# Performance work log

Hardware: AMD Instinct MI355X
Metric: run time of the kernel (lower is better)

The kernel has to match this reference:

```python
import jax, jax.numpy as jnp
import numpy as np

T, B, C = 4, 2, 128
LT, LH, LW = 8, 32, 32
NUM_HEADS = 8
HEAD_DIM = C // NUM_HEADS
THETA = 0.7
V_TH = 1.0
TAU = 2.0  # spikingjelly LIFNode default tau
N_WIN = (2, 2, 2)
TOPK = 4
EPS = 1e-5
ATAN_ALPHA = 2.0  # spikingjelly surrogate.ATan default


@jax.custom_vjp
def spike(x):
    return (x >= 0.0).astype(x.dtype)

def _spike_fwd(x):
    return spike(x), x

def _spike_bwd(x, g):
    s = (jnp.pi / 2.0) * ATAN_ALPHA * x
    return (g * (ATAN_ALPHA / 2.0) / (1.0 + s * s),)

spike.defvjp(_spike_fwd, _spike_bwd)


def lif(x_seq):
    """Multi-step LIF: v'=v+(x-v)/tau, spike at v>=V_TH, hard reset to 0 (detached)."""
    def step(v, x):
        v = v + (x - v) / TAU
        s = spike(v - V_TH)
        v = v * (1.0 - jax.lax.stop_gradient(s))  # detach_reset, v_reset=0
        return v, s
    _, s_seq = jax.lax.scan(step, jnp.zeros_like(x_seq[0]), x_seq)
    return s_seq


def bn(x, gamma, beta):
    # BatchNorm3d(track_running_stats=False) on [T*B, C, D, H, W]: batch stats per channel
    mean = x.mean(axis=(0, 1, 3, 4, 5), keepdims=True)
    var = x.var(axis=(0, 1, 3, 4, 5), keepdims=True)
    shp = (1, 1, -1, 1, 1, 1)
    return (x - mean) * jax.lax.rsqrt(var + EPS) * gamma.reshape(shp) + beta.reshape(shp)


def conv3d(x, w, pad):
    t, b = x.shape[:2]
    y = jax.lax.conv_general_dilated(
        x.reshape((t * b,) + x.shape[2:]), w,
        window_strides=(1, 1, 1), padding=[(pad, pad)] * 3,
        dimension_numbers=('NCDHW', 'OIDHW', 'NCDHW'))
    return y.reshape((t, b) + y.shape[1:])


def cdc_t(x, w):
    out = conv3d(x, w, 1)
    # central-difference temporal term: 1x1x1 conv with summed first/last temporal slices
    kd = w[:, :, 0].sum((-1, -2)) + w[:, :, 2].sum((-1, -2))  # [O, I]
    return out - THETA * jnp.einsum('oi,tbidhw->tbodhw', kd, x)


def to_wins(t):
    wt, wh, ww = N_WIN
    Tn, Bn, Cn, Lt, Lh, Lw = t.shape
    lt, lh, lw = Lt // wt, Lh // wh, Lw // ww
    t = t.reshape(Tn, Bn, Cn, wt, lt, wh, lh, ww, lw)
    t = t.transpose(0, 1, 3, 5, 7, 4, 6, 8, 2)
    return t.reshape(Tn, Bn, wt * wh * ww, lt * lh * lw, Cn)


def setup_inputs() -> dict:
    key = jax.random.key(0)
    ks = jax.random.split(key, 4)
    x = jax.random.normal(ks[0], (T, B, C, LT, LH, LW), jnp.float32)
    qw = jax.random.normal(ks[1], (C, C, 3, 3, 3), jnp.float32) / np.sqrt(C * 27)
    kw = jax.random.normal(ks[2], (C, C), jnp.float32) / np.sqrt(C)
    pw = jax.random.normal(ks[3], (C, C), jnp.float32) / np.sqrt(C)
    ones = jnp.ones((C,), jnp.float32)
    zeros = jnp.zeros((C,), jnp.float32)
    return {"x": x, "qw": qw, "q_gamma": ones, "q_beta": zeros,
            "kw": kw, "k_gamma": ones, "k_beta": zeros,
            "v_gamma": ones, "v_beta": zeros,
            "pw": pw, "p_gamma": ones, "p_beta": zeros}


def reference(x, qw, q_gamma, q_beta, kw, k_gamma, k_beta,
              v_gamma, v_beta, pw, p_gamma, p_beta):
    Tn, Bn, Cn, Lt, Lh, Lw = x.shape
    wt, wh, ww = N_WIN
    num_wins = wt * wh * ww
    lt, lh, lw = Lt // wt, Lh // wh, Lw // ww

    q_real = bn(cdc_t(x, qw), q_gamma, q_beta)
    k_real = bn(jnp.einsum('oi,tbidhw->tbodhw', kw, x), k_gamma, k_beta)

    # region-level routing from pre-spike activations
    q_region = to_wins(q_real).mean(axis=(0, 3))  # [B, W, C]
    k_region = to_wins(k_real).mean(axis=(0, 3))
    a_r = jnp.einsum('bwc,bvc->bwv', q_region, k_region) * (HEAD_DIM ** -0.5)
    k_eff = min(TOPK, num_wins)
    _, idx = jax.lax.top_k(a_r, k_eff)  # [B, W, k]

    q = lif(q_real)
    k = lif(k_real)
    v = lif(bn(x, v_gamma, v_beta))
    q_w = to_wins(q)  # [T,B,W,S,C]
    k_w = to_wins(k)
    v_w = to_wins(v)

    # gather routed windows per (batch, target window), mean-aggregate over top-k
    gather = jax.vmap(lambda src_b, idx_b: src_b[:, idx_b], in_axes=(1, 0), out_axes=1)
    k_agg = gather(k_w, idx).mean(axis=3)  # [T,B,W,S,C]
    v_agg = gather(v_w, idx).mean(axis=3)

    S = q_w.shape[3]
    q_h = q_w.reshape(Tn, Bn, num_wins, S, NUM_HEADS, HEAD_DIM)
    k_h = k_agg.reshape(Tn, Bn, num_wins, S, NUM_HEADS, HEAD_DIM)
    v_h = v_agg.reshape(Tn, Bn, num_wins, S, NUM_HEADS, HEAD_DIM)

    attn = (q_h * k_h).sum(axis=5, keepdims=True)  # [T,B,W,S,H,1]
    attn = lif(attn)
    out = (attn * v_h).reshape(Tn, Bn, num_wins, S, Cn)

    out = out.reshape(Tn, Bn, wt, wh, ww, lt, lh, lw, Cn)
    out = out.transpose(0, 1, 8, 2, 5, 3, 6, 4, 7).reshape(Tn, Bn, Cn, Lt, Lh, Lw)

    out = lif(out)
    out = bn(jnp.einsum('oi,tbidhw->tbodhw', pw, out), p_gamma, p_beta)
    return out
```

## Files before the change

kernel.cpp:

```cpp
#include <hip/hip_runtime.h>

#define TT 4
#define BB 2
#define CC 128
#define DD 8
#define HHH 32
#define WWW 32
#define PP (DD*HHH*WWW)
#define TSTRIDE (BB*CC*PP)
#define NWIN 8
#define SSS 1024
#define NHEAD 8
#define HDIM 16
#define THETA 0.7f
#define VTH 1.0f
#define NPERC (TT*BB*PP)
#define EPSf 1e-5f

typedef unsigned short ushortT;
typedef unsigned char ucharT;
typedef _Float16 half_t;
typedef _Float16 f16x8 __attribute__((ext_vector_type(8)));
typedef float    f32x16 __attribute__((ext_vector_type(16)));

typedef const __attribute__((address_space(1))) void* as1_cvp;
typedef __attribute__((address_space(3))) void* as3_vp;

__global__ __launch_bounds__(256) void prep_wmodT(const float* __restrict__ qw,
                                                  float* __restrict__ wmodT) {
    int oi = blockIdx.x*256 + threadIdx.x;
    if (oi >= CC*CC) return;
    int o  = oi >> 7;
    int ic = oi & 127;
    const float* wp = qw + (size_t)oi*27;
    float kd = 0.f;
    #pragma unroll
    for (int t=0; t<9; t++) kd += wp[t] + wp[18+t];
    #pragma unroll
    for (int t=0; t<27; t++) {
        float v = wp[t] - ((t==13) ? THETA*kd : 0.f);
        wmodT[((size_t)o*27 + t)*CC + ic] = v;
    }
}

__global__ __launch_bounds__(256) void prep_wfrag(const float* __restrict__ wmodT,
                                                  half_t* __restrict__ wfrag) {
    int id = blockIdx.x*256 + threadIdx.x;
    if (id >= 8*27*4*64) return;
    int lane = id & 63;
    int r = id >> 6;
    int m = r & 3; r >>= 2;
    int t = r % 27;
    int kb = r / 27;
    int o   = m*32 + (lane & 31);
    int ic0 = kb*16 + (lane>>5)*8;
    size_t base = ((size_t)(id>>6))*2*64*8 + (size_t)lane*8;
    #pragma unroll
    for (int j=0;j<8;j++){
        float v = wmodT[((size_t)o*27 + t)*CC + ic0 + j];
        half_t h = (half_t)v;
        half_t l = (half_t)(v - (float)h);
        wfrag[base + 0*64*8 + j] = h;
        wfrag[base + 1*64*8 + j] = l;
    }
}

__global__ __launch_bounds__(256) void prep_w1frag(const float* __restrict__ W,
                                                   half_t* __restrict__ frag) {
    int id = blockIdx.x*256 + threadIdx.x;
    if (id >= 2048) return;
    int lane = id & 63;
    int r = id >> 6;
    int m = r & 3;
    int kb = r >> 2;
    int o   = m*32 + (lane & 31);
    int ic0 = kb*16 + (lane>>5)*8;
    size_t base = ((size_t)(kb*4+m))*2*64*8 + (size_t)lane*8;
    #pragma unroll
    for (int j=0;j<8;j++){
        float v = W[(size_t)o*CC + ic0 + j];
        half_t h = (half_t)v;
        half_t l = (half_t)(v - (float)h);
        frag[base + 0*64*8 + j] = h;
        frag[base + 1*64*8 + j] = l;
    }
}

__global__ __launch_bounds__(256) void build_xsplit(const float* __restrict__ x,
                                                    half_t* __restrict__ xsp) {
    int id = blockIdx.x*256 + threadIdx.x;
    if (id >= 8*16*8*34*34) return;
    int wt = id % 34; int r = id/34;
    int hp = r % 34;  r /= 34;
    int dz = r % 8;   r /= 8;
    int icg = r & 15; int tb = r >> 4;
    bool inb = (hp>=1) & (hp<=32) & (wt>=1) & (wt<=32);
    half_t h8[8], l8[8];
    #pragma unroll
    for (int j=0;j<8;j++){
        float v = 0.f;
        if (inb)
            v = x[((size_t)(tb*CC + icg*8+j))*PP + (size_t)dz*1024 + (hp-1)*32 + (wt-1)];
        half_t h = (half_t)v;
        half_t l = (half_t)(v - (float)h);
        h8[j]=h; l8[j]=l;
    }
    #pragma unroll
    for (int sp=0; sp<2; sp++){
        size_t gu = (((((size_t)tb*2 + sp)*16 + icg)*8 + dz)*34 + hp)*34 + wt;
        half_t* dst = xsp + gu*8;
        const half_t* src = (sp==0)?h8:l8;
        #pragma unroll
        for (int j=0;j<8;j++) dst[j] = src[j];
    }
}

__global__ __launch_bounds__(512,2) void conv_mfma3(const half_t* __restrict__ xsp,
                                                    const half_t* __restrict__ wfrag,
                                                    float* __restrict__ y0,
                                                    float* __restrict__ y1) {
    extern __shared__ half_t slab[];
    int tid  = threadIdx.x;
    int wid  = tid >> 6;
    int lane = tid & 63;
    int ln   = lane & 31;
    int half_ = lane >> 5;
    int hg = blockIdx.x;
    int dp = blockIdx.y;
    int z  = blockIdx.z;
    int tb = z >> 1, kh = z & 1;
    int H0 = hg*4, d0 = dp*4;
    int r  = wid & 3;
    int q  = wid >> 2;
    float* y = kh ? y1 : y0;

    auto STAGE = [&](int bk, int bsel) {
        int kb = kh*4 + bk;
        half_t* bufp = slab + (size_t)bsel*(4896*8);
        #pragma unroll 1
        for (int k2=0; k2<10; k2++) {
            int u = tid + (k2<<9);
            if (u < 4896) {
                int sp  = (u >= 2448) ? 1 : 0;
                int r1  = u - sp*2448;
                int icg = (r1 >= 1224) ? 1 : 0;
                int p2  = r1 - icg*1224;
                int dzs = p2/204; int r3 = p2 - dzs*204;
                int hp  = r3/34;  int wt = r3 - hp*34;
                int dd  = d0 - 1 + dzs;
                const half_t* src = ((unsigned)dd < 8u)
                    ? &xsp[((((((size_t)tb*2 + sp)*16 + (kb*2+icg))*8 + dd)*34 + (H0+hp))*34 + wt)*8]
                    : &xsp[(size_t)ln*8];
                __builtin_amdgcn_global_load_lds((as1_cvp)src,
                    (as3_vp)(bufp + (size_t)u*8), 16, 0, 0);
            }
        }
    };

    f32x16 acc[2][4];
    #pragma unroll
    for (int dt=0;dt<2;dt++)
        #pragma unroll
        for (int m=0;m<4;m++)
            #pragma unroll
            for (int i=0;i<16;i++) acc[dt][m][i] = 0.f;

    f16x8 ca[4][2];
    #pragma unroll
    for (int m=0;m<4;m++)
        #pragma unroll
        for (int sp=0;sp<2;sp++)
            ca[m][sp] = *(const f16x8*)&wfrag[((((size_t)(kh*4*27)*4 + m)*2+sp)*64 + lane)*8];

    asm volatile("" ::: "memory");
    STAGE(0,0);
    STAGE(1,1);
    asm volatile("" ::: "memory");

    #pragma unroll 1
    for (int kk=0; kk<4; kk++) {
        int kb = kh*4 + kk;
        if (kk == 0) {
            if (wid < 5) asm volatile("s_waitcnt vmcnt(10)" ::: "memory");
            else         asm volatile("s_waitcnt vmcnt(9)"  ::: "memory");
        } else {
            asm volatile("s_waitcnt vmcnt(63)" ::: "memory");
        }
        __builtin_amdgcn_s_barrier();
        asm volatile("" ::: "memory");
        const half_t* bufp = slab + (size_t)(kk&1)*(4896*8);
        #pragma unroll 1
        for (int t=0; t<27; t++) {
            int dz=t/9; int rr=t-dz*9; int dh=rr/3; int dw=rr-dh*3;
            f16x8 cb[2][2];
            #pragma unroll
            for (int dt=0;dt<2;dt++){
                int unitb = (q*2 + dt + dz)*204 + (r+dh)*34 + (ln+dw);
                #pragma unroll
                for (int sp=0;sp<2;sp++)
                    cb[dt][sp] = *(const f16x8*)&bufp[(size_t)((sp*2+half_)*1224 + unitb)*8];
            }
            f16x8 na[4][2];
            int nt  = (t<26)? t+1 : 0;
            int nkb = (t<26)? kb  : ((kk<3)? kb+1 : kb);
            #pragma unroll
            for (int m=0;m<4;m++)
                #pragma unroll
                for (int sp=0;sp<2;sp++)
                    na[m][sp] = *(const f16x8*)&wfrag[((((size_t)(nkb*27+nt)*4+m)*2+sp)*64 + lane)*8];
            #pragma unroll
            for (int dt=0;dt<2;dt++)
                #pragma unroll
                for (int m=0;m<4;m++) acc[dt][m] = __builtin_amdgcn_mfma_f32_32x32x16_f16(ca[m][0], cb[dt][0], acc[dt][m],0,0,0);
            #pragma unroll
            for (int dt=0;dt<2;dt++)
                #pragma unroll
                for (int m=0;m<4;m++) acc[dt][m] = __builtin_amdgcn_mfma_f32_32x32x16_f16(ca[m][0], cb[dt][1], acc[dt][m],0,0,0);
            #pragma unroll
            for (int dt=0;dt<2;dt++)
                #pragma unroll
                for (int m=0;m<4;m++) acc[dt][m] = __builtin_amdgcn_mfma_f32_32x32x16_f16(ca[m][1], cb[dt][0], acc[dt][m],0,0,0);
            #pragma unroll
            for (int m=0;m<4;m++)
                #pragma unroll
                for (int sp=0;sp<2;sp++) ca[m][sp] = na[m][sp];
        }
        asm volatile("" ::: "memory");
        __builtin_amdgcn_s_barrier();
        asm volatile("" ::: "memory");
        if (kk < 2) STAGE(kk+2, kk&1);
    }

    int h = H0 + r;
    #pragma unroll
    for (int dt=0; dt<2; dt++) {
        int d = d0 + q*2 + dt;
        #pragma unroll
        for (int m=0; m<4; m++) {
            #pragma unroll
            for (int reg=0; reg<16; reg++) {
                int row = (reg&3) + 8*(reg>>2) + 4*half_;
                int o = m*32 + row;
                y[((size_t)tb*CC + o)*PP + d*1024 + h*32 + ln] = acc[dt][m][reg];
            }
        }
    }
}

__global__ __launch_bounds__(256) void kgemm_mfma(const half_t* __restrict__ xsp,
                                                  const half_t* __restrict__ wk,
                                                  float* __restrict__ y) {
    int tid  = threadIdx.x;
    int wid  = tid >> 6;
    int lane = tid & 63;
    int ln   = lane & 31;
    int half_ = lane >> 5;
    int hg = blockIdx.x, d = blockIdx.y, tb = blockIdx.z;
    int h = hg*4 + wid;

    f32x16 acc[4];
    #pragma unroll
    for (int m=0;m<4;m++)
        #pragma unroll
        for (int i=0;i<16;i++) acc[m][i] = 0.f;

    #pragma unroll 2
    for (int kb=0; kb<8; kb++) {
        f16x8 b[2];
        #pragma unroll
        for (int sp=0; sp<2; sp++) {
            size_t gu = (((((size_t)tb*2 + sp)*16 + (kb*2+half_))*8 + d)*34 + (h+1))*34 + (ln+1);
            b[sp] = *(const f16x8*)&xsp[gu*8];
        }
        #pragma unroll
        for (int m=0; m<4; m++) {
            const half_t* wb = wk + ((size_t)(kb*4+m))*2*64*8 + (size_t)lane*8;
            f16x8 a0 = *(const f16x8*)&wb[0*64*8];
            f16x8 a1 = *(const f16x8*)&wb[1*64*8];
            acc[m] = __builtin_amdgcn_mfma_f32_32x32x16_f16(a0, b[0], acc[m],0,0,0);
            acc[m] = __builtin_amdgcn_mfma_f32_32x32x16_f16(a0, b[1], acc[m],0,0,0);
            acc[m] = __builtin_amdgcn_mfma_f32_32x32x16_f16(a1, b[0], acc[m],0,0,0);
        }
    }
    #pragma unroll
    for (int m=0; m<4; m++) {
        #pragma unroll
        for (int reg=0; reg<16; reg++) {
            int row = (reg&3) + 8*(reg>>2) + 4*half_;
            int o = m*32 + row;
            y[((size_t)tb*CC + o)*PP + d*1024 + h*32 + ln] = acc[m][reg];
        }
    }
}

__global__ __launch_bounds__(256) void pgemm_mfma(const ushortT* __restrict__ spkb,
                                                  const half_t* __restrict__ wp,
                                                  float* __restrict__ y) {
    int tid  = threadIdx.x;
    int wid  = tid >> 6;
    int lane = tid & 63;
    int ln   = lane & 31;
    int half_ = lane >> 5;
    int hg = blockIdx.x, d = blockIdx.y, tb = blockIdx.z;
    int h = hg*4 + wid;
    int p = d*1024 + h*32 + ln;

    f32x16 acc[4];
    #pragma unroll
    for (int m=0;m<4;m++)
        #pragma unroll
        for (int i=0;i<16;i++) acc[m][i] = 0.f;

    #pragma unroll 2
    for (int kb=0; kb<8; kb++) {
        f16x8 b = *(const f16x8*)&spkb[(((size_t)tb*16 + (kb*2+half_))*PP + p)*8];
        #pragma unroll
        for (int m=0; m<4; m++) {
            const half_t* wb = wp + ((size_t)(kb*4+m))*2*64*8 + (size_t)lane*8;
            f16x8 a0 = *(const f16x8*)&wb[0*64*8];
            f16x8 a1 = *(const f16x8*)&wb[1*64*8];
            acc[m] = __builtin_amdgcn_mfma_f32_32x32x16_f16(a0, b, acc[m],0,0,0);
            acc[m] = __builtin_amdgcn_mfma_f32_32x32x16_f16(a1, b, acc[m],0,0,0);
        }
    }
    #pragma unroll
    for (int m=0; m<4; m++) {
        #pragma unroll
        for (int reg=0; reg<16; reg++) {
            int row = (reg&3) + 8*(reg>>2) + 4*half_;
            int o = m*32 + row;
            y[((size_t)tb*CC + o)*PP + p] = acc[m][reg];
        }
    }
}

__global__ __launch_bounds__(128) void win_stats(const float* __restrict__ q0,
        const float* __restrict__ q1,
        const float* __restrict__ k, const float* __restrict__ x,
        float* __restrict__ rsum, float* __restrict__ rsq) {
    int blk = blockIdx.x;
    int src = blk >> 11;
    int r   = blk & 2047;
    const float* base = (src==0) ? q0 : ((src==1) ? k : x);
    int c  = r & 127;
    int wi = (r >> 7) & 7;
    int b  = r >> 10;
    int wd = wi>>2, wh = (wi>>1)&1, ww = wi&1;
    int tid = threadIdx.x;
    float s=0.f, s2=0.f;
    for (int t=0;t<TT;t++){
        size_t off0 = ((size_t)(t*BB+b)*CC + c)*PP;
        const float* p  = base + off0;
        const float* p2 = q1 + off0;
        for (int si=tid; si<SSS; si+=128){
            int ld = si>>8, lh=(si>>4)&15, lw=si&15;
            int o = ((wd*4+ld)<<10) + ((wh*16+lh)<<5) + (ww*16+lw);
            float v = p[o];
            if (src==0) v += p2[o];
            s += v; s2 += v*v;
        }
    }
    __shared__ float ls[128], ls2[128];
    ls[tid]=s; ls2[tid]=s2; __syncthreads();
    for (int off=64;off>0;off>>=1){
        if(tid<off){ ls[tid]+=ls[tid+off]; ls2[tid]+=ls2[tid+off]; }
        __syncthreads();
    }
    if (tid==0){ rsum[blk]=ls[0]; rsq[blk]=ls2[0]; }
}

__global__ __launch_bounds__(384) void route_fin(const float* __restrict__ rsum,
        const float* __restrict__ rsq,
        const float* __restrict__ qg, const float* __restrict__ qb,
        const float* __restrict__ kg, const float* __restrict__ kb,
        float* __restrict__ stats, int* __restrict__ idxout) {
    __shared__ float qn[16*128], kn[16*128], ar[16*8];
    __shared__ float csum[384], csq[384];
    int tid = threadIdx.x;
    {
        int src = tid >> 7, c = tid & 127;
        float s=0.f, s2=0.f;
        for (int bw=0; bw<16; bw++){
            int idx = src*2048 + bw*128 + c;
            s  += rsum[idx];
            s2 += rsq[idx];
        }
        stats[src*256 + c]       = s;
        stats[src*256 + 128 + c] = s2;
        csum[tid]=s; csq[tid]=s2;
    }
    __syncthreads();
    for (int e=tid; e<16*128; e+=384){
        int c = e&127;
        float qm = csum[c]*(1.f/NPERC);
        float qv = csq[c]*(1.f/NPERC) - qm*qm;
        float qr = rsqrtf(qv + EPSf);
        qn[e] = (rsum[e]*(1.f/(TT*SSS)) - qm)*qr*qg[c] + qb[c];
        float km = csum[128+c]*(1.f/NPERC);
        float kv = csq[128+c]*(1.f/NPERC) - km*km;
        float kr = rsqrtf(kv + EPSf);
        kn[e] = (rsum[2048+e]*(1.f/(TT*SSS)) - km)*kr*kg[c] + kb[c];
    }
    __syncthreads();
    if (tid < 128){
        int b = tid>>6, w=(tid>>3)&7, v=tid&7;
        float s=0.f;
        for (int c=0;c<128;c++) s += qn[(b*8+w)*128+c]*kn[(b*8+v)*128+c];
        ar[(b*8+w)*8+v] = s * 0.25f;
    }
    __syncthreads();
    if (tid < 16){
        const float* row = &ar[tid*8];
        bool used[8] = {false,false,false,false,false,false,false,false};
        for (int j=0;j<4;j++){
            int best=0; float bv=-3.0e38f;
            for (int v=0; v<8; v++){
                if (!used[v] && row[v] > bv){ bv=row[v]; best=v; }
            }
            used[best]=true;
            idxout[tid*4+j]=best;
        }
    }
}

__global__ __launch_bounds__(256) void lif_bn_win3(const float* __restrict__ q0,
        const float* __restrict__ q1,
        const float* __restrict__ kin, const float* __restrict__ xin,
        ucharT* __restrict__ qs, ucharT* __restrict__ ks, ucharT* __restrict__ vs,
        const float* __restrict__ stats,
        const float* __restrict__ qg, const float* __restrict__ qb,
        const float* __restrict__ kg, const float* __restrict__ kb,
        const float* __restrict__ vg, const float* __restrict__ vb) {
    int src = blockIdx.y;
    const float* in  = (src==0) ? q0 : ((src==1) ? kin : xin);
    ucharT*      spk = (src==0) ? qs  : ((src==1) ? ks  : vs);
    const float* gamma = (src==0) ? qg : ((src==1) ? kg : vg);
    const float* beta  = (src==0) ? qb : ((src==1) ? kb : vb);
    int e = blockIdx.x*256 + threadIdx.x;
    if (e >= BB*CC*PP) return;
    int p = e & (PP-1);
    int c = (e >> 13) & 127;
    int b = e >> 20;
    float mean = stats[src*256 + c]*(1.f/NPERC);
    float var  = stats[src*256 + 128 + c]*(1.f/NPERC) - mean*mean;
    float sc = rsqrtf(var+EPSf)*gamma[c];
    float sh = beta[c] - mean*sc;
    int d = p>>10, h=(p>>5)&31, w=p&31;
    int wi = ((d>>2)*2 + (h>>4))*2 + (w>>4);
    int si = (((d&3)<<4) + (h&15))*16 + (w&15);
    size_t widx = ((size_t)(b*NWIN+wi)*CC + c)*SSS + si;
    float v=0.f;
    #pragma unroll
    for (int t=0;t<TT;t++){
        size_t ti = (size_t)t*TSTRIDE + e;
        float raw = in[ti];
        if (src==0) raw += q1[ti];
        float xn = raw*sc + sh;
        v = (v+xn)*0.5f;
        float s = (v>=VTH)?1.f:0.f;
        spk[(size_t)t*TSTRIDE + widx] = (ucharT)(v>=VTH ? 1 : 0);
        v *= (1.f - s);
    }
}

__global__ __launch_bounds__(256) void attn_lif(const ucharT* __restrict__ qspk,
        const ucharT* __restrict__ kspk, const ucharT* __restrict__ vspk,
        const int* __restrict__ idx, ushortT* __restrict__ spkb) {
    int id = blockIdx.x*256 + threadIdx.x;
    if (id >= BB*NWIN*NHEAD*SSS) return;
    int s  = id & 1023;
    int hh = (id>>10) & 7;
    int wi = (id>>13) & 7;
    int b  = id>>16;
    int bw = b*NWIN+wi;
    size_t qbase = ((size_t)bw*CC + hh*HDIM)*SSS + s;
    size_t sbase[4];
    #pragma unroll
    for (int j=0;j<4;j++){
        int src = idx[bw*4+j];
        sbase[j] = ((size_t)(b*NWIN+src)*CC + hh*HDIM)*SSS + s;
    }
    int wd = wi>>2, wh = (wi>>1)&1, ww = wi&1;
    int d3 = wd*4 + (s>>8), h3 = wh*16 + ((s>>4)&15), w3 = ww*16 + (s&15);
    int p  = (d3<<10) + (h3<<5) + w3;

    float v=0.f;
    float v2[16];
    #pragma unroll
    for (int dd=0; dd<16; dd++) v2[dd]=0.f;

    #pragma unroll 1
    for (int t=0;t<TT;t++){
        size_t toff = (size_t)t*TSTRIDE;
        int km[16], vm[16];
        #pragma unroll
        for (int dd=0;dd<16;dd++){ km[dd]=0; vm[dd]=0; }
        #pragma unroll
        for (int j=0;j<4;j++){
            const ucharT* kp = kspk+toff+sbase[j];
            const ucharT* vp = vspk+toff+sbase[j];
            #pragma unroll
            for (int dd=0; dd<16; dd++){
                km[dd] += kp[(size_t)dd*SSS];
                vm[dd] += vp[(size_t)dd*SSS];
            }
        }
        const ucharT* qp = qspk+toff+qbase;
        int atti=0;
        #pragma unroll
        for (int dd=0;dd<16;dd++) atti += (int)qp[(size_t)dd*SSS]*km[dd];
        float att = (float)atti * 0.25f;
        v = (v+att)*0.5f;
        float sp = (v>=VTH)?1.f:0.f;
        v *= (1.f-sp);
        float spq = sp*0.25f;
        union { ushortT u[8]; uint4 q4; } pk0, pk1;
        #pragma unroll
        for (int dd=0;dd<16;dd++){
            float ov = spq*(float)vm[dd];
            v2[dd] = (v2[dd]+ov)*0.5f;
            float s2 = (v2[dd]>=VTH)?1.f:0.f;
            v2[dd] *= (1.f-s2);
            ushortT bs = (s2 != 0.f) ? (ushortT)0x3C00 : (ushortT)0;
            if (dd < 8) pk0.u[dd] = bs; else pk1.u[dd-8] = bs;
        }
        int tb2 = t*BB + b;
        size_t base = (((size_t)tb2*16 + hh*2)*PP + p)*8;
        *(uint4*)&spkb[base] = pk0.q4;
        *(uint4*)&spkb[base + (size_t)PP*8] = pk1.q4;
    }
}

__global__ __launch_bounds__(256) void pstats_part(const float* __restrict__ xin,
        float* __restrict__ part_sum, float* __restrict__ part_sq) {
    int blk = blockIdx.x;
    int c = blk & 127, tb = blk >> 7;
    int tid = threadIdx.x;
    const float* p = xin + ((size_t)tb*CC + c)*PP;
    float s=0.f, s2=0.f;
    for (int i=tid; i<PP; i+=256){ float v=p[i]; s+=v; s2+=v*v; }
    __shared__ float ls[256], ls2[256];
    ls[tid]=s; ls2[tid]=s2; __syncthreads();
    for (int off=128; off>0; off>>=1){
        if (tid<off){ ls[tid]+=ls[tid+off]; ls2[tid]+=ls2[tid+off]; }
        __syncthreads();
    }
    if (tid==0){ part_sum[blk]=ls[0]; part_sq[blk]=ls2[0]; }
}

__global__ __launch_bounds__(256) void bn_apply(const float* __restrict__ xin,
        float* __restrict__ yout,
        const float* __restrict__ part_sum, const float* __restrict__ part_sq,
        const float* __restrict__ gamma, const float* __restrict__ beta) {
    size_t i = (size_t)blockIdx.x*256 + threadIdx.x;
    if (i >= (size_t)TT*BB*CC*PP) return;
    int c = (int)((i>>13)&127);
    float s=0.f, s2=0.f;
    #pragma unroll
    for (int tb=0; tb<8; tb++){
        s  += part_sum[tb*128+c];
        s2 += part_sq[tb*128+c];
    }
    float mean = s*(1.f/NPERC);
    float var  = s2*(1.f/NPERC) - mean*mean;
    float sc = rsqrtf(var+EPSf)*gamma[c];
    float sh = beta[c] - mean*sc;
    yout[i] = xin[i]*sc + sh;
}

extern "C" void kernel_launch(void* const* d_in, const int* in_sizes, int n_in,
                              void* d_out, int out_size, void* d_ws, size_t ws_size,
                              hipStream_t stream) {
    const float* x  = (const float*)d_in[0];
    const float* qw = (const float*)d_in[1];
    const float* qg = (const float*)d_in[2];
    const float* qb = (const float*)d_in[3];
    const float* kw = (const float*)d_in[4];
    const float* kg = (const float*)d_in[5];
    const float* kb = (const float*)d_in[6];
    const float* vg = (const float*)d_in[7];
    const float* vb = (const float*)d_in[8];
    const float* pw = (const float*)d_in[9];
    const float* pg = (const float*)d_in[10];
    const float* pb = (const float*)d_in[11];
    float* out = (float*)d_out;
    float* ws  = (float*)d_ws;

    const size_t NEL = (size_t)TT*TSTRIDE;
    float* part0 = ws;
    float* part1 = ws + NEL;
    half_t* xsp  = (half_t*)(ws + 2*NEL);
    const size_t KCONV_OFF = 2*NEL + 10747904;
    float* kconv = ws + KCONV_OFF;
    float* wf_base = ws + KCONV_OFF + NEL;
    half_t* wfrag  = (half_t*)wf_base;
    half_t* wkfrag = (half_t*)(wf_base + 442368);
    float*  wmodT  = wf_base + 442368 + 16384;
    float* stats = ws + 5*NEL;
    float* rsum = stats + 1024;
    float* rsq  = rsum + 6144;
    float* ppart_sum = rsq + 6144;
    float* ppart_sq  = ppart_sum + 1024;
    int*   idxp = (int*)(ppart_sq + 1024);

    ucharT* qspk = (ucharT*)(ws + 2*NEL);
    ucharT* kspk = (ucharT*)(ws + 2*NEL) + 8388608;
    ucharT* vspk = (ucharT*)(ws + 2*NEL) + 16777216;
    ushortT* spkb  = (ushortT*)ws;
    half_t* wpfrag = (half_t*)(ws + NEL);
    float*  pconv  = ws + KCONV_OFF;

    prep_wmodT<<<64,256,0,stream>>>(qw, wmodT);
    prep_wfrag<<<216,256,0,stream>>>(wmodT, wfrag);
    prep_w1frag<<<8,256,0,stream>>>(kw, wkfrag);
    build_xsplit<<<4624,256,0,stream>>>(x, xsp);
    {
        static bool attr_set = false;
        const int shmem = 2*4896*8*(int)sizeof(half_t);
        if (!attr_set) {
            hipFuncSetAttribute((const void*)conv_mfma3,
                                hipFuncAttributeMaxDynamicSharedMemorySize, shmem);
            attr_set = true;
        }
        dim3 cg(8,2,16);
        conv_mfma3<<<cg,512,shmem,stream>>>(xsp, wfrag, part0, part1);
    }
    {
        dim3 gg(8,8,8);
        kgemm_mfma<<<gg,256,0,stream>>>(xsp, wkfrag, kconv);
    }
    win_stats<<<6144,128,0,stream>>>(part0, part1, kconv, x, rsum, rsq);
    route_fin<<<1,384,0,stream>>>(rsum, rsq, qg,qb,kg,kb, stats, idxp);
    {
        dim3 lg(8192,3);
        lif_bn_win3<<<lg,256,0,stream>>>(part0,part1,kconv,x,
                                         qspk,kspk,vspk,
                                         stats, qg,qb,kg,kb,vg,vb);
    }
    attn_lif<<<512,256,0,stream>>>(qspk,kspk,vspk,idxp,spkb);
    prep_w1frag<<<8,256,0,stream>>>(pw, wpfrag);
    {
        dim3 gg(8,8,8);
        pgemm_mfma<<<gg,256,0,stream>>>(spkb, wpfrag, pconv);
    }
    pstats_part<<<1024,256,0,stream>>>(pconv, ppart_sum, ppart_sq);
    bn_apply<<<32768,256,0,stream>>>(pconv, out, ppart_sum, ppart_sq, pg, pb);
}
```

Baseline: 396.8 us.

## Retile conv warps to 4 depth x 2 channel blocks; merge weight-frag prep launches

The conv kernel's per-warp tile changes from 2 depth slices x 4 output-channel blocks to 4 depth slices x 2 output-channel blocks. Each warp now loads half as many weight fragments from global memory per tap but reads twice as many B operands from LDS. The goal is to cut global and L2 weight traffic, at the cost of more LDS reads per MFMA. The key and projection 1x1 weight-fragment preparation is also merged into one launch, which moves the projection fragments to a separate workspace region and removes one kernel launch.

Result: no change. 393.5 us (-0.8%).

```diff
diff --git a/kernel.cpp b/kernel.cpp
--- a/kernel.cpp
+++ b/kernel.cpp
@@ -65,12 +65,17 @@
     }
 }
 
-__global__ __launch_bounds__(256) void prep_w1frag(const float* __restrict__ W,
-                                                   half_t* __restrict__ frag) {
+__global__ __launch_bounds__(256) void prep_w1frag2(const float* __restrict__ Wk,
+                                                    const float* __restrict__ Wp,
+                                                    half_t* __restrict__ fragk,
+                                                    half_t* __restrict__ fragp) {
     int id = blockIdx.x*256 + threadIdx.x;
-    if (id >= 2048) return;
-    int lane = id & 63;
-    int r = id >> 6;
+    if (id >= 4096) return;
+    const float* W    = (id < 2048) ? Wk : Wp;
+    half_t*      frag = (id < 2048) ? fragk : fragp;
+    int i2 = id & 2047;
+    int lane = i2 & 63;
+    int r = i2 >> 6;
     int m = r & 3;
     int kb = r >> 2;
     int o   = m*32 + (lane & 31);
@@ -131,7 +136,7 @@
     int tb = z >> 1, kh = z & 1;
     int H0 = hg*4, d0 = dp*4;
     int r  = wid & 3;
-    int q  = wid >> 2;
+    int mh = wid >> 2;
     float* y = kh ? y1 : y0;
 
     auto STAGE = [&](int bk, int bsel) {
@@ -157,20 +162,20 @@
         }
     };
 
-    f32x16 acc[2][4];
-    #pragma unroll
-    for (int dt=0;dt<2;dt++)
-        #pragma unroll
-        for (int m=0;m<4;m++)
-            #pragma unroll
-            for (int i=0;i<16;i++) acc[dt][m][i] = 0.f;
-
-    f16x8 ca[4][2];
-    #pragma unroll
-    for (int m=0;m<4;m++)
+    f32x16 acc[4][2];
+    #pragma unroll
+    for (int dt=0;dt<4;dt++)
+        #pragma unroll
+        for (int mm=0;mm<2;mm++)
+            #pragma unroll
+            for (int i=0;i<16;i++) acc[dt][mm][i] = 0.f;
+
+    f16x8 ca[2][2];
+    #pragma unroll
+    for (int mm=0;mm<2;mm++)
         #pragma unroll
         for (int sp=0;sp<2;sp++)
-            ca[m][sp] = *(const f16x8*)&wfrag[((((size_t)(kh*4*27)*4 + m)*2+sp)*64 + lane)*8];
+            ca[mm][sp] = *(const f16x8*)&wfrag[((((size_t)(kh*4*27)*4 + (mh*2+mm))*2+sp)*64 + lane)*8];
 
     asm volatile("" ::: "memory");
     STAGE(0,0);
@@ -192,38 +197,38 @@
         #pragma unroll 1
         for (int t=0; t<27; t++) {
             int dz=t/9; int rr=t-dz*9; int dh=rr/3; int dw=rr-dh*3;
-            f16x8 cb[2][2];
-            #pragma unroll
-            for (int dt=0;dt<2;dt++){
-                int unitb = (q*2 + dt + dz)*204 + (r+dh)*34 + (ln+dw);
+            f16x8 cb[4][2];
+            #pragma unroll
+            for (int dt=0;dt<4;dt++){
+                int unitb = (dt + dz)*204 + (r+dh)*34 + (ln+dw);
                 #pragma unroll
                 for (int sp=0;sp<2;sp++)
                     cb[dt][sp] = *(const f16x8*)&bufp[(size_t)((sp*2+half_)*1224 + unitb)*8];
             }
-            f16x8 na[4][2];
+            f16x8 na[2][2];
             int nt  = (t<26)? t+1 : 0;
             int nkb = (t<26)? kb  : ((kk<3)? kb+1 : kb);
             #pragma unroll
-            for (int m=0;m<4;m++)
+            for (int mm=0;mm<2;mm++)
                 #pragma unroll
                 for (int sp=0;sp<2;sp++)
-                    na[m][sp] = *(const f16x8*)&wfrag[((((size_t)(nkb*27+nt)*4+m)*2+sp)*64 + lane)*8];
-            #pragma unroll
-            for (int dt=0;dt<2;dt++)
+                    na[mm][sp] = *(const f16x8*)&wfrag[((((size_t)(nkb*27+nt)*4+(mh*2+mm))*2+sp)*64 + lane)*8];
+            #pragma unroll
+            for (int dt=0;dt<4;dt++)
                 #pragma unroll
-                for (int m=0;m<4;m++) acc[dt][m] = __builtin_amdgcn_mfma_f32_32x32x16_f16(ca[m][0], cb[dt][0], acc[dt][m],0,0,0);
-            #pragma unroll
-            for (int dt=0;dt<2;dt++)
+                for (int mm=0;mm<2;mm++) acc[dt][mm] = __builtin_amdgcn_mfma_f32_32x32x16_f16(ca[mm][0], cb[dt][0], acc[dt][mm],0,0,0);
+            #pragma unroll
+            for (int dt=0;dt<4;dt++)
                 #pragma unroll
-                for (int m=0;m<4;m++) acc[dt][m] = __builtin_amdgcn_mfma_f32_32x32x16_f16(ca[m][0], cb[dt][1], acc[dt][m],0,0,0);
-            #pragma unroll
-            for (int dt=0;dt<2;dt++)
+                for (int mm=0;mm<2;mm++) acc[dt][mm] = __builtin_amdgcn_mfma_f32_32x32x16_f16(ca[mm][0], cb[dt][1], acc[dt][mm],0,0,0);
+            #pragma unroll
+            for (int dt=0;dt<4;dt++)
                 #pragma unroll
-                for (int m=0;m<4;m++) acc[dt][m] = __builtin_amdgcn_mfma_f32_32x32x16_f16(ca[m][1], cb[dt][0], acc[dt][m],0,0,0);
-            #pragma unroll
-            for (int m=0;m<4;m++)
+                for (int mm=0;mm<2;mm++) acc[dt][mm] = __builtin_amdgcn_mfma_f32_32x32x16_f16(ca[mm][1], cb[dt][0], acc[dt][mm],0,0,0);
+            #pragma unroll
+            for (int mm=0;mm<2;mm++)
                 #pragma unroll
-                for (int sp=0;sp<2;sp++) ca[m][sp] = na[m][sp];
+                for (int sp=0;sp<2;sp++) ca[mm][sp] = na[mm][sp];
         }
         asm volatile("" ::: "memory");
         __builtin_amdgcn_s_barrier();
@@ -233,15 +238,15 @@
 
     int h = H0 + r;
     #pragma unroll
-    for (int dt=0; dt<2; dt++) {
-        int d = d0 + q*2 + dt;
-        #pragma unroll
-        for (int m=0; m<4; m++) {
+    for (int dt=0; dt<4; dt++) {
+        int d = d0 + dt;
+        #pragma unroll
+        for (int mm=0; mm<2; mm++) {
             #pragma unroll
             for (int reg=0; reg<16; reg++) {
                 int row = (reg&3) + 8*(reg>>2) + 4*half_;
-                int o = m*32 + row;
-                y[((size_t)tb*CC + o)*PP + d*1024 + h*32 + ln] = acc[dt][m][reg];
+                int o = (mh*2+mm)*32 + row;
+                y[((size_t)tb*CC + o)*PP + d*1024 + h*32 + ln] = acc[dt][mm][reg];
             }
         }
     }
@@ -596,6 +601,7 @@
     half_t* wfrag  = (half_t*)wf_base;
     half_t* wkfrag = (half_t*)(wf_base + 442368);
     float*  wmodT  = wf_base + 442368 + 16384;
+    half_t* wpfrag = (half_t*)(wf_base + 442368 + 16384 + 442368);
     float* stats = ws + 5*NEL;
     float* rsum = stats + 1024;
     float* rsq  = rsum + 6144;
@@ -607,12 +613,11 @@
     ucharT* kspk = (ucharT*)(ws + 2*NEL) + 8388608;
     ucharT* vspk = (ucharT*)(ws + 2*NEL) + 16777216;
     ushortT* spkb  = (ushortT*)ws;
-    half_t* wpfrag = (half_t*)(ws + NEL);
     float*  pconv  = ws + KCONV_OFF;
 
     prep_wmodT<<<64,256,0,stream>>>(qw, wmodT);
     prep_wfrag<<<216,256,0,stream>>>(wmodT, wfrag);
-    prep_w1frag<<<8,256,0,stream>>>(kw, wkfrag);
+    prep_w1frag2<<<16,256,0,stream>>>(kw, pw, wkfrag, wpfrag);
     build_xsplit<<<4624,256,0,stream>>>(x, xsp);
     {
         static bool attr_set = false;
@@ -638,7 +643,6 @@
                                          stats, qg,qb,kg,kb,vg,vb);
     }
     attn_lif<<<512,256,0,stream>>>(qspk,kspk,vspk,idxp,spkb);
-    prep_w1frag<<<8,256,0,stream>>>(pw, wpfrag);
     {
         dim3 gg(8,8,8);
         pgemm_mfma<<<gg,256,0,stream>>>(spkb, wpfrag, pconv);
```
